# Kernel optimization log

Measured on AMD Instinct MI355X. Metric: run time of the kernel, lower is better.

Reference implementation:

```python
import jax, jax.numpy as jnp
import numpy as np

D = 256
RANK = 64
H = 8
DH = D // H
TOPK = 32  # top-k survivors per query row
NEG = -1e9


def lowrank(x, u, v):
    # x:[...,d] @ u:[d,rank] @ v:[rank,d]
    return (x @ u) @ v


def setup_inputs() -> dict:
    key = jax.random.key(0)
    ks = jax.random.split(key, 13)
    s_u = 1.0 / np.sqrt(D)
    s_v = 1.0 / np.sqrt(RANK)

    def pu(k):
        return jax.random.normal(k, (D, RANK), jnp.float32) * s_u

    def pv(k):
        return jax.random.normal(k, (RANK, D), jnp.float32) * s_v

    return {
        "x": jax.random.normal(ks[0], (2, 2048, D), jnp.float32),
        "ne_u": pu(ks[1]), "ne_v": pv(ks[2]),
        "wq_u": pu(ks[3]), "wq_v": pv(ks[4]),
        "wk_u": pu(ks[5]), "wk_v": pv(ks[6]),
        "wv_u": pu(ks[7]), "wv_v": pv(ks[8]),
        "wo_u": pu(ks[9]), "wo_v": pv(ks[10]),
        "es_u": pu(ks[11]), "es_v": pv(ks[12]),
    }


def reference(x, ne_u, ne_v, wq_u, wq_v, wk_u, wk_v, wv_u, wv_v, wo_u, wo_v, es_u, es_v):
    B, N, _ = x.shape
    # node embedding (low-rank projection)
    h = lowrank(x, ne_u, ne_v)  # [B,N,d]

    # low-rank multi-head Q/K/V
    def heads(t):  # [B,N,d] -> [B,H,N,dh]
        return t.reshape(B, N, H, DH).transpose(0, 2, 1, 3)

    q = heads(lowrank(h, wq_u, wq_v))
    k = heads(lowrank(h, wk_u, wk_v))
    v = heads(lowrank(h, wv_u, wv_v))

    scores = jnp.einsum("bhnd,bhmd->bhnm", q, k) / jnp.sqrt(jnp.float32(DH))
    # top-k sparsification per query row
    kth = jax.lax.top_k(scores, TOPK)[0][..., -1:]  # [B,H,N,1]
    masked = jnp.where(scores >= kth, scores, NEG)
    attn = jax.nn.softmax(masked, axis=-1)  # [B,H,N,N]

    out = jnp.einsum("bhnm,bhmd->bhnd", attn, v)  # [B,H,N,dh]
    out = out.transpose(0, 2, 1, 3).reshape(B, N, D)
    h2 = lowrank(out, wo_u, wo_v)  # output projection

    # edge scores -> adjacency with sigmoid + zero diagonal epilogue
    el = lowrank(h2, es_u, es_v)  # [B,N,d]
    adjacency = jax.nn.sigmoid(jnp.einsum("bnd,bmd->bnm", el, el))
    adjacency = adjacency * (1.0 - jnp.eye(N, dtype=adjacency.dtype))
    return adjacency, attn
```

## Files before the change

### kernel.cpp

```cpp
#include <hip/hip_runtime.h>
#include <hip/hip_bf16.h>
#include <cstdint>
#include <cstddef>

#define ATTN_OFF (2u*2048u*2048u)
#define SLOTS 48
#define DELTA 1e-3f
#define MAXB 16
#define CCAP 96

typedef __attribute__((ext_vector_type(8))) short bf16x8;
typedef __attribute__((ext_vector_type(4))) float f32x4;

__device__ __forceinline__ unsigned short bf16_hi(float f) {
  __hip_bfloat16 h = __float2bfloat16(f);
  return *(unsigned short*)&h;
}
__device__ __forceinline__ float bf16_val(unsigned short u) {
  __hip_bfloat16 h = *(__hip_bfloat16*)&u;
  return __bfloat162float(h);
}

template <typename InT, int MODE>
__global__ __launch_bounds__(256) void lowrank_kernel(
    const InT* __restrict__ in, const float* __restrict__ u,
    const float* __restrict__ vw, void* __restrict__ out0,
    void* __restrict__ out1, void* __restrict__ out2, double scale) {
  __shared__ double mid[4][64];
  int tid = threadIdx.x;
  int rr = tid >> 6;
  int j  = tid & 63;
  int row = blockIdx.x * 4 + rr;

  const InT* inr = in + (size_t)row * 256;
  double a0 = 0, a1 = 0, a2 = 0, a3 = 0;
#pragma unroll 8
  for (int k4 = 0; k4 < 64; ++k4) {
    int kk = k4 * 4;
    a0 = fma((double)inr[kk + 0], (double)u[(kk + 0) * 64 + j], a0);
    a1 = fma((double)inr[kk + 1], (double)u[(kk + 1) * 64 + j], a1);
    a2 = fma((double)inr[kk + 2], (double)u[(kk + 2) * 64 + j], a2);
    a3 = fma((double)inr[kk + 3], (double)u[(kk + 3) * 64 + j], a3);
  }
  mid[rr][j] = (a0 + a1) + (a2 + a3);
  __syncthreads();

#pragma unroll
  for (int cc = 0; cc < 4; ++cc) {
    int col = j + 64 * cc;
    double o0 = 0, o1 = 0, o2 = 0, o3 = 0;
#pragma unroll 4
    for (int r4 = 0; r4 < 16; ++r4) {
      int r = r4 * 4;
      o0 = fma(mid[rr][r + 0], (double)vw[(r + 0) * 256 + col], o0);
      o1 = fma(mid[rr][r + 1], (double)vw[(r + 1) * 256 + col], o1);
      o2 = fma(mid[rr][r + 2], (double)vw[(r + 2) * 256 + col], o2);
      o3 = fma(mid[rr][r + 3], (double)vw[(r + 3) * 256 + col], o3);
    }
    double o = (o0 + o1) + (o2 + o3);
    if (MODE == 0) {
      ((double*)out0)[(size_t)row * 256 + col] = o;
    } else if (MODE == 1) {
      ((float*)out0)[(size_t)row * 256 + col] = (float)o;
    } else {
      ((double*)out0)[(size_t)row * 256 + col] = o;
      int b = row >> 11, m = row & 2047, hh = col >> 5, d = col & 31;
      size_t addr = (((size_t)(b * 8 + hh)) * 2048 + m) * 32 + d;
      float f = (float)(o * scale);
      unsigned short hi = bf16_hi(f);
      float lof = f - bf16_val(hi);
      ((unsigned short*)out1)[addr] = hi;
      ((unsigned short*)out2)[addr] = bf16_hi(lof);
    }
  }
}

__global__ __launch_bounds__(512, 4) void attn_kernel(
    const unsigned short* __restrict__ qh, const unsigned short* __restrict__ ql,
    const unsigned short* __restrict__ kh, const unsigned short* __restrict__ kl,
    const double* __restrict__ qd, const double* __restrict__ kd,
    float* __restrict__ attn, float* __restrict__ pval,
    unsigned short* __restrict__ pidx) {
  __shared__ unsigned hist[16][256];
  __shared__ float cand[16][CCAP];
  __shared__ float rowmax_s[16][8];
  __shared__ float zpart_s[16][8];
  __shared__ float mx_s[16];
  __shared__ float kth_s[16];
  __shared__ float zinv_s[16];
  __shared__ int   kB_s[16];
  __shared__ unsigned kneed_s[16];
  __shared__ unsigned ccnt[16];
  __shared__ unsigned scnt[16];
  __shared__ unsigned chi_s[16];
  __shared__ unsigned bcnt[16];
  __shared__ unsigned short bidx[16][MAXB];
  __shared__ unsigned short bkeep[16][MAXB];
  __shared__ double bs64[16][MAXB];

  int tid = threadIdx.x;
  int bx  = blockIdx.x;
  int slab = bx >> 7;
  int rowtile = bx & 127;
  int b = slab >> 3, hh = slab & 7;
  int w = tid >> 6;
  int l = tid & 63;
  int g = l >> 4;
  int li = l & 15;
  const double INV64 = 0.17677669529663688110021109052621;

  size_t qoff = (((size_t)slab * 2048 + rowtile * 16 + li) * 32) + g * 8;
  bf16x8 a_hi = *(const bf16x8*)(qh + qoff);
  bf16x8 a_lo = *(const bf16x8*)(ql + qoff);

  float s[16][4];
  size_t kbase = ((size_t)slab * 2048 + w * 256 + li) * 32 + g * 8;
#pragma unroll
  for (int tt = 0; tt < 16; ++tt) {
    bf16x8 b_hi = *(const bf16x8*)(kh + kbase + (size_t)tt * 512);
    bf16x8 b_lo = *(const bf16x8*)(kl + kbase + (size_t)tt * 512);
    f32x4 acc = {0.f, 0.f, 0.f, 0.f};
    acc = __builtin_amdgcn_mfma_f32_16x16x32_bf16(a_hi, b_hi, acc, 0, 0, 0);
    acc = __builtin_amdgcn_mfma_f32_16x16x32_bf16(a_hi, b_lo, acc, 0, 0, 0);
    acc = __builtin_amdgcn_mfma_f32_16x16x32_bf16(a_lo, b_hi, acc, 0, 0, 0);
#pragma unroll
    for (int reg = 0; reg < 4; ++reg) s[tt][reg] = acc[reg];
  }

  for (int i = tid; i < 16 * 256; i += 512) ((unsigned*)hist)[i] = 0u;
  if (tid < 16) {
    ccnt[tid] = 0u; scnt[tid] = 0u; chi_s[tid] = 0u; bcnt[tid] = 0u;
    kth_s[tid] = -1e30f; kB_s[tid] = -1;
  }
  size_t prow0 = ((size_t)slab * 2048 + rowtile * 16);
  for (int i = tid; i < 16 * SLOTS; i += 512) {
    pval[prow0 * SLOTS + i] = 0.0f;
    pidx[prow0 * SLOTS + i] = 0;
  }
  {
    float lmx[4];
#pragma unroll
    for (int reg = 0; reg < 4; ++reg) {
      float m = s[0][reg];
#pragma unroll
      for (int tt = 1; tt < 16; ++tt) m = fmaxf(m, s[tt][reg]);
      lmx[reg] = m;
    }
#pragma unroll
    for (int off = 1; off < 16; off <<= 1) {
#pragma unroll
      for (int reg = 0; reg < 4; ++reg)
        lmx[reg] = fmaxf(lmx[reg], __shfl_xor(lmx[reg], (unsigned)off, 16));
    }
    if (li == 0) {
#pragma unroll
      for (int reg = 0; reg < 4; ++reg) rowmax_s[4 * g + reg][w] = lmx[reg];
    }
  }
  __syncthreads();

  if (tid < 16) {
    float m = rowmax_s[tid][0];
#pragma unroll
    for (int i = 1; i < 8; ++i) m = fmaxf(m, rowmax_s[tid][i]);
    mx_s[tid] = m;
  }
  __syncthreads();

#pragma unroll
  for (int reg = 0; reg < 4; ++reg) {
    int rloc = 4 * g + reg;
    float mx = mx_s[rloc];
#pragma unroll
    for (int tt = 0; tt < 16; ++tt) {
      int bb = (int)((mx - s[tt][reg]) * 16.0f);
      bb = bb > 255 ? 255 : bb;
      atomicAdd(&hist[rloc][bb], 1u);
    }
  }
  __syncthreads();

  if (w < 4) {
    int rloc = w * 4 + g;
    unsigned cnt16 = 0;
#pragma unroll
    for (int i = 0; i < 16; ++i) cnt16 += hist[rloc][li * 16 + i];
    unsigned pre = cnt16;
#pragma unroll
    for (int off = 1; off < 16; off <<= 1) {
      unsigned t = __shfl_up(pre, (unsigned)off, 16);
      if (li >= off) pre += t;
    }
    unsigned excl = pre - cnt16;
    bool flag = (excl < 32u) && (pre >= 32u);
    unsigned long long bal = __ballot(flag);
    unsigned seg = (unsigned)((bal >> (g * 16)) & 0xFFFFull);
    if (flag) {
      int src = __ffs(seg) - 1;
      if (li == src) {
        unsigned cum = excl;
        int B = 255; unsigned cb = 0;
#pragma unroll
        for (int i = 0; i < 16; ++i) {
          unsigned hv = hist[rloc][li * 16 + i];
          if (cum < 32u && cum + hv >= 32u) { B = li * 16 + i; cb = cum; }
          cum += hv;
        }
        kB_s[rloc] = B;
        kneed_s[rloc] = 32u - cb;
      }
    }
  }
  __syncthreads();

#pragma unroll
  for (int reg = 0; reg < 4; ++reg) {
    int rloc = 4 * g + reg;
    float mx = mx_s[rloc];
    int kB = kB_s[rloc];
#pragma unroll
    for (int tt = 0; tt < 16; ++tt) {
      int bb = (int)((mx - s[tt][reg]) * 16.0f);
      bb = bb > 255 ? 255 : bb;
      if (bb == kB) {
        unsigned slot = atomicAdd(&ccnt[rloc], 1u);
        if (slot < (unsigned)CCAP) cand[rloc][slot] = s[tt][reg];
      }
    }
  }
  __syncthreads();

  if (w < 4) {
    int rloc = w * 4 + g;
    unsigned n0 = ccnt[rloc];
    n0 = n0 > (unsigned)CCAP ? (unsigned)CCAP : n0;
    unsigned need = kneed_s[rloc];
    if (need > n0) need = n0;
    for (unsigned ci = (unsigned)li; ci < n0; ci += 16u) {
      float x = cand[rloc][ci];
      unsigned r = 0;
      for (unsigned jj = 0; jj < n0; ++jj) {
        float y = cand[rloc][jj];
        r += (y > x || (y == x && jj < ci)) ? 1u : 0u;
      }
      if (r == need - 1u) kth_s[rloc] = x;
    }
  }
  __syncthreads();

#pragma unroll
  for (int reg = 0; reg < 4; ++reg) {
    int rloc = 4 * g + reg;
    float kth = kth_s[rloc];
    unsigned cnt = 0;
#pragma unroll
    for (int tt = 0; tt < 16; ++tt) {
      float v = s[tt][reg];
      if (v > kth + DELTA) {
        ++cnt;
      } else if (!(v < kth - DELTA)) {
        unsigned slot = atomicAdd(&bcnt[rloc], 1u);
        if (slot < (unsigned)MAXB)
          bidx[rloc][slot] = (unsigned short)(w * 256 + tt * 16 + li);
      }
    }
#pragma unroll
    for (int off = 1; off < 16; off <<= 1)
      cnt += (unsigned)__shfl_xor((int)cnt, off, 16);
    if (li == 0) atomicAdd(&chi_s[rloc], cnt);
  }
  __syncthreads();

  if (w < 4) {
    int rloc = w * 4 + g;
    unsigned bn = bcnt[rloc];
    bn = bn > (unsigned)MAXB ? (unsigned)MAXB : bn;
    const double* qrow =
        qd + ((size_t)(b * 2048 + rowtile * 16 + rloc)) * 256 + hh * 32;
    for (unsigned ci = (unsigned)li; ci < bn; ci += 16u) {
      int m = bidx[rloc][ci];
      const double* krow = kd + ((size_t)(b * 2048 + m)) * 256 + hh * 32;
      double acc = 0.0;
#pragma unroll 8
      for (int d = 0; d < 32; ++d) acc = fma(qrow[d], krow[d], acc);
      bs64[rloc][ci] = acc * INV64;
    }
    unsigned need2 = 32u - chi_s[rloc];
    for (unsigned ci = (unsigned)li; ci < bn; ci += 16u) {
      double x = bs64[rloc][ci];
      unsigned r = 0;
      for (unsigned jj = 0; jj < bn; ++jj)
        r += (bs64[rloc][jj] > x) ? 1u : 0u;
      bkeep[rloc][ci] = (r < need2) ? 1 : 0;
    }
  }
  __syncthreads();

  {
    float zs[4];
#pragma unroll
    for (int reg = 0; reg < 4; ++reg) {
      int rloc = 4 * g + reg;
      float mx = mx_s[rloc], kth = kth_s[rloc];
      unsigned bn = bcnt[rloc];
      bn = bn > (unsigned)MAXB ? (unsigned)MAXB : bn;
      float z = 0.0f;
#pragma unroll
      for (int tt = 0; tt < 16; ++tt) {
        float v = s[tt][reg];
        bool keep;
        if (v > kth + DELTA) {
          keep = true;
        } else if (v < kth - DELTA) {
          keep = false;
        } else {
          unsigned short col = (unsigned short)(w * 256 + tt * 16 + li);
          keep = (v >= kth);
          for (unsigned jj = 0; jj < bn; ++jj) {
            if (bidx[rloc][jj] == col) { keep = bkeep[rloc][jj] != 0; break; }
          }
        }
        float p = keep ? __expf(v - mx) : 0.0f;
        s[tt][reg] = p;
        z += p;
      }
      zs[reg] = z;
    }
#pragma unroll
    for (int off = 1; off < 16; off <<= 1) {
#pragma unroll
      for (int reg = 0; reg < 4; ++reg)
        zs[reg] += __shfl_xor(zs[reg], (unsigned)off, 16);
    }
    if (li == 0) {
#pragma unroll
      for (int reg = 0; reg < 4; ++reg) zpart_s[4 * g + reg][w] = zs[reg];
    }
  }
  __syncthreads();

  if (tid < 16) {
    float z = 0.0f;
#pragma unroll
    for (int i = 0; i < 8; ++i) z += zpart_s[tid][i];
    zinv_s[tid] = 1.0f / z;
  }
  __syncthreads();

#pragma unroll
  for (int reg = 0; reg < 4; ++reg) {
    int rloc = 4 * g + reg;
    float rz = zinv_s[rloc];
    float* pr = attn + (prow0 + rloc) * 2048 + w * 256 + li;
    float* pvr = pval + (prow0 + rloc) * SLOTS;
    unsigned short* pir = pidx + (prow0 + rloc) * SLOTS;
#pragma unroll
    for (int tt = 0; tt < 16; ++tt) {
      float p = s[tt][reg];
      float pn = p * rz;
      pr[tt * 16] = pn;
      if (p > 0.0f) {
        unsigned slot = atomicAdd(&scnt[rloc], 1u);
        if (slot < (unsigned)SLOTS) {
          pvr[slot] = pn;
          pir[slot] = (unsigned short)(w * 256 + tt * 16 + li);
        }
      }
    }
  }
}

__global__ __launch_bounds__(256) void pv_sparse_kernel(
    const float* __restrict__ pval, const unsigned short* __restrict__ pidx,
    const float* __restrict__ v, float* __restrict__ out) {
  __shared__ float vals[8][SLOTS];
  __shared__ unsigned short idxs[8][SLOTS];
  int tid = threadIdx.x;
  int grp = blockIdx.x;
  int slab = grp >> 8;
  int rg = grp & 255;
  int b = slab >> 3, hh = slab & 7;
  int r = tid >> 5, dh = tid & 31;

  for (int e = tid; e < 8 * SLOTS; e += 256) {
    int rr = e / SLOTS, ii = e % SLOTS;
    size_t base = ((size_t)slab * 2048 + rg * 8 + rr) * SLOTS + ii;
    vals[rr][ii] = pval[base];
    idxs[rr][ii] = pidx[base];
  }
  __syncthreads();

  const float* vb = v + (size_t)b * 2048 * 256 + hh * 32 + dh;
  float acc = 0.0f;
#pragma unroll 4
  for (int i = 0; i < SLOTS; ++i) {
    float p = vals[r][i];
    int m = idxs[r][i];
    acc = fmaf(p, vb[(size_t)m * 256], acc);
  }
  int n = rg * 8 + r;
  out[((size_t)(b * 2048 + n)) * 256 + hh * 32 + dh] = acc;
}

__global__ __launch_bounds__(256) void adj_kernel(const float* __restrict__ el,
                                                  float* __restrict__ adj) {
  __shared__ float a_lds[64][33];
  __shared__ float b_lds[64][33];
  int tid = threadIdx.x;
  int b = blockIdx.z, rt = blockIdx.y, ct = blockIdx.x;
  const float* elb = el + (size_t)b * 2048 * 256;
  int tr = tid >> 4, tc = tid & 15;
  float acc[4][4] = {};

  for (int kt = 0; kt < 8; ++kt) {
    __syncthreads();
#pragma unroll
    for (int jj = 0; jj < 8; ++jj) {
      int e = tid + 256 * jj;
      int r = e >> 5, d = e & 31;
      a_lds[r][d] = elb[(size_t)(rt * 64 + r) * 256 + kt * 32 + d];
      b_lds[r][d] = elb[(size_t)(ct * 64 + r) * 256 + kt * 32 + d];
    }
    __syncthreads();
#pragma unroll
    for (int kk = 0; kk < 32; ++kk) {
      float va[4], vb[4];
#pragma unroll
      for (int i = 0; i < 4; ++i) {
        va[i] = a_lds[tr * 4 + i][kk];
        vb[i] = b_lds[tc * 4 + i][kk];
      }
#pragma unroll
      for (int i = 0; i < 4; ++i)
#pragma unroll
        for (int j2 = 0; j2 < 4; ++j2)
          acc[i][j2] = fmaf(va[i], vb[j2], acc[i][j2]);
    }
  }
#pragma unroll
  for (int i = 0; i < 4; ++i) {
    int rg = rt * 64 + tr * 4 + i;
#pragma unroll
    for (int j2 = 0; j2 < 4; ++j2) {
      int cg = ct * 64 + tc * 4 + j2;
      float sg = 1.0f / (1.0f + expf(-acc[i][j2]));
      if (rg == cg) sg = 0.0f;
      adj[((size_t)b * 2048 + rg) * 2048 + cg] = sg;
    }
  }
}

extern "C" void kernel_launch(void* const* d_in, const int* in_sizes, int n_in,
                              void* d_out, int out_size, void* d_ws,
                              size_t ws_size, hipStream_t stream) {
  const float* x    = (const float*)d_in[0];
  const float* ne_u = (const float*)d_in[1];
  const float* ne_v = (const float*)d_in[2];
  const float* wq_u = (const float*)d_in[3];
  const float* wq_v = (const float*)d_in[4];
  const float* wk_u = (const float*)d_in[5];
  const float* wk_v = (const float*)d_in[6];
  const float* wv_u = (const float*)d_in[7];
  const float* wv_v = (const float*)d_in[8];
  const float* wo_u = (const float*)d_in[9];
  const float* wo_v = (const float*)d_in[10];
  const float* es_u = (const float*)d_in[11];
  const float* es_v = (const float*)d_in[12];

  float* adj  = (float*)d_out;
  float* attn = adj + (size_t)ATTN_OFF;

  char* ws = (char*)d_ws;
  double* h  = (double*)(ws);
  double* qd = (double*)(ws + ((size_t)8  << 20));
  double* kd = (double*)(ws + ((size_t)16 << 20));
  unsigned short* qh = (unsigned short*)(ws + ((size_t)24 << 20));
  unsigned short* ql = (unsigned short*)(ws + ((size_t)26 << 20));
  unsigned short* kh = (unsigned short*)(ws + ((size_t)28 << 20));
  unsigned short* kl = (unsigned short*)(ws + ((size_t)30 << 20));
  float* v    = (float*)(ws + ((size_t)32 << 20));
  unsigned short* pidx = (unsigned short*)(ws + ((size_t)36 << 20));
  float* pval = (float*)(ws);
  float* out  = (float*)(ws + ((size_t)8  << 20));
  float* h2   = (float*)(ws + ((size_t)12 << 20));
  float* el   = (float*)(ws + ((size_t)16 << 20));

  const double INV = 0.17677669529663688110021109052621;

  lowrank_kernel<float,  0><<<1024, 256, 0, stream>>>(x, ne_u, ne_v, h, nullptr, nullptr, 1.0);
  lowrank_kernel<double, 3><<<1024, 256, 0, stream>>>(h, wq_u, wq_v, qd, qh, ql, INV);
  lowrank_kernel<double, 3><<<1024, 256, 0, stream>>>(h, wk_u, wk_v, kd, kh, kl, 1.0);
  lowrank_kernel<double, 1><<<1024, 256, 0, stream>>>(h, wv_u, wv_v, v, nullptr, nullptr, 1.0);

  attn_kernel<<<2048, 512, 0, stream>>>(qh, ql, kh, kl, qd, kd, attn, pval, pidx);
  pv_sparse_kernel<<<4096, 256, 0, stream>>>(pval, pidx, v, out);

  lowrank_kernel<float, 1><<<1024, 256, 0, stream>>>(out, wo_u, wo_v, h2, nullptr, nullptr, 1.0);
  lowrank_kernel<float, 1><<<1024, 256, 0, stream>>>(h2, es_u, es_v, el, nullptr, nullptr, 1.0);

  adj_kernel<<<dim3(32, 32, 2), 256, 0, stream>>>(el, adj);
}
```

Before: 438.5 us.

## Fuse node-embed and QKV projections; compute adjacency GEMM with split-bf16 MFMA

The node-embedding low-rank projection and the three Q/K/V projections now run in one kernel that keeps each row's h in shared memory, so the double-precision h buffer is no longer written and read back. The edge-score projection now emits bf16 hi/lo pairs, and the adjacency GEMM uses 16x16x32 bf16 MFMA instructions with three products (hi*hi, hi*lo, lo*hi) to approximate fp32 precision, replacing the scalar LDS-tiled FMA loop. The sigmoid switches to fast __expf. The split-bf16 scheme and fast exp can shift adjacency values slightly relative to fp32, and the MFMA kernel reads its operands straight from global memory without LDS staging.

```diff
diff --git a/kernel.cpp b/kernel.cpp
--- a/kernel.cpp
+++ b/kernel.cpp
@@ -21,11 +21,117 @@
   return __bfloat162float(h);
 }
 
+__global__ __launch_bounds__(256) void fused_qkv_kernel(
+    const float* __restrict__ x, const float* __restrict__ ne_u,
+    const float* __restrict__ ne_v, const float* __restrict__ wq_u,
+    const float* __restrict__ wq_v, const float* __restrict__ wk_u,
+    const float* __restrict__ wk_v, const float* __restrict__ wv_u,
+    const float* __restrict__ wv_v, double* __restrict__ qd,
+    double* __restrict__ kd, unsigned short* __restrict__ qh,
+    unsigned short* __restrict__ ql, unsigned short* __restrict__ kh,
+    unsigned short* __restrict__ kl, float* __restrict__ v) {
+  __shared__ double xm[4][64];
+  __shared__ double hrow[4][256];
+  __shared__ double mid2[4][64];
+
+  int tid = threadIdx.x;
+  int rr = tid >> 6;
+  int j  = tid & 63;
+  int row = blockIdx.x * 4 + rr;
+  int b = row >> 11, m = row & 2047;
+  const double INV = 0.17677669529663688110021109052621;
+
+  const float* xr = x + (size_t)row * 256;
+  {
+    double a0 = 0, a1 = 0, a2 = 0, a3 = 0;
+#pragma unroll 8
+    for (int k4 = 0; k4 < 64; ++k4) {
+      int kk = k4 * 4;
+      a0 = fma((double)xr[kk + 0], (double)ne_u[(kk + 0) * 64 + j], a0);
+      a1 = fma((double)xr[kk + 1], (double)ne_u[(kk + 1) * 64 + j], a1);
+      a2 = fma((double)xr[kk + 2], (double)ne_u[(kk + 2) * 64 + j], a2);
+      a3 = fma((double)xr[kk + 3], (double)ne_u[(kk + 3) * 64 + j], a3);
+    }
+    xm[rr][j] = (a0 + a1) + (a2 + a3);
+  }
+  __syncthreads();
+
+#pragma unroll
+  for (int cc = 0; cc < 4; ++cc) {
+    int col = j + 64 * cc;
+    double o0 = 0, o1 = 0, o2 = 0, o3 = 0;
+#pragma unroll 4
+    for (int r4 = 0; r4 < 16; ++r4) {
+      int r = r4 * 4;
+      o0 = fma(xm[rr][r + 0], (double)ne_v[(r + 0) * 256 + col], o0);
+      o1 = fma(xm[rr][r + 1], (double)ne_v[(r + 1) * 256 + col], o1);
+      o2 = fma(xm[rr][r + 2], (double)ne_v[(r + 2) * 256 + col], o2);
+      o3 = fma(xm[rr][r + 3], (double)ne_v[(r + 3) * 256 + col], o3);
+    }
+    hrow[rr][col] = (o0 + o1) + (o2 + o3);
+  }
+  __syncthreads();
+
+  for (int p = 0; p < 3; ++p) {
+    const float* pu = (p == 0) ? wq_u : (p == 1) ? wk_u : wv_u;
+    const float* pw = (p == 0) ? wq_v : (p == 1) ? wk_v : wv_v;
+
+    double a0 = 0, a1 = 0, a2 = 0, a3 = 0;
+#pragma unroll 8
+    for (int k4 = 0; k4 < 64; ++k4) {
+      int kk = k4 * 4;
+      a0 = fma(hrow[rr][kk + 0], (double)pu[(kk + 0) * 64 + j], a0);
+      a1 = fma(hrow[rr][kk + 1], (double)pu[(kk + 1) * 64 + j], a1);
+      a2 = fma(hrow[rr][kk + 2], (double)pu[(kk + 2) * 64 + j], a2);
+      a3 = fma(hrow[rr][kk + 3], (double)pu[(kk + 3) * 64 + j], a3);
+    }
+    mid2[rr][j] = (a0 + a1) + (a2 + a3);
+    __syncthreads();
+
+#pragma unroll
+    for (int cc = 0; cc < 4; ++cc) {
+      int col = j + 64 * cc;
+      double o0 = 0, o1 = 0, o2 = 0, o3 = 0;
+#pragma unroll 4
+      for (int r4 = 0; r4 < 16; ++r4) {
+        int r = r4 * 4;
+        o0 = fma(mid2[rr][r + 0], (double)pw[(r + 0) * 256 + col], o0);
+        o1 = fma(mid2[rr][r + 1], (double)pw[(r + 1) * 256 + col], o1);
+        o2 = fma(mid2[rr][r + 2], (double)pw[(r + 2) * 256 + col], o2);
+        o3 = fma(mid2[rr][r + 3], (double)pw[(r + 3) * 256 + col], o3);
+      }
+      double o = (o0 + o1) + (o2 + o3);
+      if (p == 2) {
+        v[(size_t)row * 256 + col] = (float)o;
+      } else {
+        int hh = col >> 5, d = col & 31;
+        size_t haddr = (((size_t)(b * 8 + hh)) * 2048 + m) * 32 + d;
+        if (p == 0) {
+          qd[(size_t)row * 256 + col] = o;
+          float f = (float)(o * INV);
+          unsigned short hi = bf16_hi(f);
+          float lof = f - bf16_val(hi);
+          qh[haddr] = hi;
+          ql[haddr] = bf16_hi(lof);
+        } else {
+          kd[(size_t)row * 256 + col] = o;
+          float f = (float)o;
+          unsigned short hi = bf16_hi(f);
+          float lof = f - bf16_val(hi);
+          kh[haddr] = hi;
+          kl[haddr] = bf16_hi(lof);
+        }
+      }
+    }
+    __syncthreads();
+  }
+}
+
 template <typename InT, int MODE>
 __global__ __launch_bounds__(256) void lowrank_kernel(
     const InT* __restrict__ in, const float* __restrict__ u,
     const float* __restrict__ vw, void* __restrict__ out0,
-    void* __restrict__ out1, void* __restrict__ out2, double scale) {
+    void* __restrict__ out1, void* __restrict__ out2) {
   __shared__ double mid[4][64];
   int tid = threadIdx.x;
   int rr = tid >> 6;
@@ -58,19 +164,14 @@
       o3 = fma(mid[rr][r + 3], (double)vw[(r + 3) * 256 + col], o3);
     }
     double o = (o0 + o1) + (o2 + o3);
-    if (MODE == 0) {
-      ((double*)out0)[(size_t)row * 256 + col] = o;
-    } else if (MODE == 1) {
+    if constexpr (MODE == 1) {
       ((float*)out0)[(size_t)row * 256 + col] = (float)o;
     } else {
-      ((double*)out0)[(size_t)row * 256 + col] = o;
-      int b = row >> 11, m = row & 2047, hh = col >> 5, d = col & 31;
-      size_t addr = (((size_t)(b * 8 + hh)) * 2048 + m) * 32 + d;
-      float f = (float)(o * scale);
+      float f = (float)o;
       unsigned short hi = bf16_hi(f);
       float lof = f - bf16_val(hi);
-      ((unsigned short*)out1)[addr] = hi;
-      ((unsigned short*)out2)[addr] = bf16_hi(lof);
+      ((unsigned short*)out1)[(size_t)row * 256 + col] = hi;
+      ((unsigned short*)out2)[(size_t)row * 256 + col] = bf16_hi(lof);
     }
   }
 }
@@ -402,48 +503,47 @@
   out[((size_t)(b * 2048 + n)) * 256 + hh * 32 + dh] = acc;
 }
 
-__global__ __launch_bounds__(256) void adj_kernel(const float* __restrict__ el,
-                                                  float* __restrict__ adj) {
-  __shared__ float a_lds[64][33];
-  __shared__ float b_lds[64][33];
+__global__ __launch_bounds__(256) void adj_mfma_kernel(
+    const unsigned short* __restrict__ elh, const unsigned short* __restrict__ ell,
+    float* __restrict__ adj) {
   int tid = threadIdx.x;
+  int l = tid & 63, w = tid >> 6;
+  int li = l & 15, g = l >> 4;
   int b = blockIdx.z, rt = blockIdx.y, ct = blockIdx.x;
-  const float* elb = el + (size_t)b * 2048 * 256;
-  int tr = tid >> 4, tc = tid & 15;
-  float acc[4][4] = {};
-
-  for (int kt = 0; kt < 8; ++kt) {
-    __syncthreads();
-#pragma unroll
-    for (int jj = 0; jj < 8; ++jj) {
-      int e = tid + 256 * jj;
-      int r = e >> 5, d = e & 31;
-      a_lds[r][d] = elb[(size_t)(rt * 64 + r) * 256 + kt * 32 + d];
-      b_lds[r][d] = elb[(size_t)(ct * 64 + r) * 256 + kt * 32 + d];
-    }
-    __syncthreads();
-#pragma unroll
-    for (int kk = 0; kk < 32; ++kk) {
-      float va[4], vb[4];
-#pragma unroll
-      for (int i = 0; i < 4; ++i) {
-        va[i] = a_lds[tr * 4 + i][kk];
-        vb[i] = b_lds[tc * 4 + i][kk];
-      }
-#pragma unroll
-      for (int i = 0; i < 4; ++i)
-#pragma unroll
-        for (int j2 = 0; j2 < 4; ++j2)
-          acc[i][j2] = fmaf(va[i], vb[j2], acc[i][j2]);
-    }
-  }
-#pragma unroll
-  for (int i = 0; i < 4; ++i) {
-    int rg = rt * 64 + tr * 4 + i;
-#pragma unroll
-    for (int j2 = 0; j2 < 4; ++j2) {
-      int cg = ct * 64 + tc * 4 + j2;
-      float sg = 1.0f / (1.0f + expf(-acc[i][j2]));
+
+  int arow = rt * 64 + w * 16 + li;
+  size_t abase = ((size_t)(b * 2048 + arow)) * 256 + g * 8;
+  size_t bbase = ((size_t)(b * 2048 + ct * 64 + li)) * 256 + g * 8;
+
+  f32x4 acc0 = {0.f, 0.f, 0.f, 0.f};
+  f32x4 acc1 = {0.f, 0.f, 0.f, 0.f};
+  f32x4 acc2 = {0.f, 0.f, 0.f, 0.f};
+  f32x4 acc3 = {0.f, 0.f, 0.f, 0.f};
+
+#pragma unroll
+  for (int kc = 0; kc < 8; ++kc) {
+    bf16x8 a_hi = *(const bf16x8*)(elh + abase + kc * 32);
+    bf16x8 a_lo = *(const bf16x8*)(ell + abase + kc * 32);
+#pragma unroll
+    for (int t = 0; t < 4; ++t) {
+      bf16x8 b_hi = *(const bf16x8*)(elh + bbase + (size_t)t * 16 * 256 + kc * 32);
+      bf16x8 b_lo = *(const bf16x8*)(ell + bbase + (size_t)t * 16 * 256 + kc * 32);
+      f32x4* pa = (t == 0) ? &acc0 : (t == 1) ? &acc1 : (t == 2) ? &acc2 : &acc3;
+      *pa = __builtin_amdgcn_mfma_f32_16x16x32_bf16(a_hi, b_hi, *pa, 0, 0, 0);
+      *pa = __builtin_amdgcn_mfma_f32_16x16x32_bf16(a_hi, b_lo, *pa, 0, 0, 0);
+      *pa = __builtin_amdgcn_mfma_f32_16x16x32_bf16(a_lo, b_hi, *pa, 0, 0, 0);
+    }
+  }
+
+  int orow0 = rt * 64 + w * 16 + g * 4;
+#pragma unroll
+  for (int t = 0; t < 4; ++t) {
+    f32x4 a = (t == 0) ? acc0 : (t == 1) ? acc1 : (t == 2) ? acc2 : acc3;
+    int cg = ct * 64 + t * 16 + li;
+#pragma unroll
+    for (int i = 0; i < 4; ++i) {
+      int rg = orow0 + i;
+      float sg = 1.0f / (1.0f + __expf(-a[i]));
       if (rg == cg) sg = 0.0f;
       adj[((size_t)b * 2048 + rg) * 2048 + cg] = sg;
     }
@@ -471,32 +571,29 @@
   float* attn = adj + (size_t)ATTN_OFF;
 
   char* ws = (char*)d_ws;
-  double* h  = (double*)(ws);
-  double* qd = (double*)(ws + ((size_t)8  << 20));
-  double* kd = (double*)(ws + ((size_t)16 << 20));
-  unsigned short* qh = (unsigned short*)(ws + ((size_t)24 << 20));
-  unsigned short* ql = (unsigned short*)(ws + ((size_t)26 << 20));
-  unsigned short* kh = (unsigned short*)(ws + ((size_t)28 << 20));
-  unsigned short* kl = (unsigned short*)(ws + ((size_t)30 << 20));
-  float* v    = (float*)(ws + ((size_t)32 << 20));
-  unsigned short* pidx = (unsigned short*)(ws + ((size_t)36 << 20));
-  float* pval = (float*)(ws);
-  float* out  = (float*)(ws + ((size_t)8  << 20));
-  float* h2   = (float*)(ws + ((size_t)12 << 20));
-  float* el   = (float*)(ws + ((size_t)16 << 20));
-
-  const double INV = 0.17677669529663688110021109052621;
-
-  lowrank_kernel<float,  0><<<1024, 256, 0, stream>>>(x, ne_u, ne_v, h, nullptr, nullptr, 1.0);
-  lowrank_kernel<double, 3><<<1024, 256, 0, stream>>>(h, wq_u, wq_v, qd, qh, ql, INV);
-  lowrank_kernel<double, 3><<<1024, 256, 0, stream>>>(h, wk_u, wk_v, kd, kh, kl, 1.0);
-  lowrank_kernel<double, 1><<<1024, 256, 0, stream>>>(h, wv_u, wv_v, v, nullptr, nullptr, 1.0);
+  double* qd = (double*)(ws);
+  double* kd = (double*)(ws + ((size_t)8  << 20));
+  unsigned short* qh = (unsigned short*)(ws + ((size_t)16 << 20));
+  unsigned short* ql = (unsigned short*)(ws + ((size_t)18 << 20));
+  unsigned short* kh = (unsigned short*)(ws + ((size_t)20 << 20));
+  unsigned short* kl = (unsigned short*)(ws + ((size_t)22 << 20));
+  float* v    = (float*)(ws + ((size_t)24 << 20));
+  float* pval = (float*)(ws + ((size_t)28 << 20));
+  unsigned short* pidx = (unsigned short*)(ws + ((size_t)35 << 20));
+  float* out  = (float*)(ws);
+  float* h2   = (float*)(ws + ((size_t)4  << 20));
+  unsigned short* elh = (unsigned short*)(ws + ((size_t)8  << 20));
+  unsigned short* ell = (unsigned short*)(ws + ((size_t)10 << 20));
+
+  fused_qkv_kernel<<<1024, 256, 0, stream>>>(
+      x, ne_u, ne_v, wq_u, wq_v, wk_u, wk_v, wv_u, wv_v,
+      qd, kd, qh, ql, kh, kl, v);
 
   attn_kernel<<<2048, 512, 0, stream>>>(qh, ql, kh, kl, qd, kd, attn, pval, pidx);
   pv_sparse_kernel<<<4096, 256, 0, stream>>>(pval, pidx, v, out);
 
-  lowrank_kernel<float, 1><<<1024, 256, 0, stream>>>(out, wo_u, wo_v, h2, nullptr, nullptr, 1.0);
-  lowrank_kernel<float, 1><<<1024, 256, 0, stream>>>(h2, es_u, es_v, el, nullptr, nullptr, 1.0);
-
-  adj_kernel<<<dim3(32, 32, 2), 256, 0, stream>>>(el, adj);
-}
+  lowrank_kernel<float, 1><<<1024, 256, 0, stream>>>(out, wo_u, wo_v, h2, nullptr, nullptr);
+  lowrank_kernel<float, 4><<<1024, 256, 0, stream>>>(h2, es_u, es_v, nullptr, elh, ell);
+
+  adj_mfma_kernel<<<dim3(32, 32, 2), 256, 0, stream>>>(elh, ell, adj);
+}
```

New measurement: 417.7 us. 4.8% less time.
